# Kernel optimization log

Measured on AMD Instinct MI355X. Metric: run time of the kernel, lower is better.

## Reference

```python
import jax, jax.numpy as jnp
import numpy as np

B, H, SQ, SKV, D, TOPK = 1, 16, 1024, 4096, 128, 64


def setup_inputs() -> dict:
    key = jax.random.key(0)
    kq, kk, kv, ki, ks = jax.random.split(key, 5)
    q = jax.random.normal(kq, (B, H, SQ, D), dtype=jnp.float32)
    k = jax.random.normal(kk, (B, H, SKV, D), dtype=jnp.float32)
    v = jax.random.normal(kv, (B, H, SKV, D), dtype=jnp.float32)
    topk_indices = jax.random.randint(ki, (B, SQ, TOPK), 0, SKV, dtype=jnp.int32)
    topk_scores = jax.random.uniform(ks, (B, SQ, TOPK), dtype=jnp.float32)
    return {"q": q, "k": k, "v": v, "topk_indices": topk_indices,
            "topk_scores": topk_scores}


def reference(q, k, v, topk_indices, topk_scores):
    # q: (b,h,s,d); k,v: (b,h,S,d) global (cp_world_size=1 all-gather is identity)
    head_dim = q.shape[-1]
    scale = head_dim ** -0.5
    # Gather selected K/V per query without dense (b,h,s,S,d) expansion.
    # idx: (b,1,s,topk,1) broadcast against (b,h,1,S,d) along axis=3.
    idx = topk_indices[:, None, :, :, None]
    k_g = jnp.take_along_axis(k[:, :, None, :, :], idx, axis=3)  # (b,h,s,t,d)
    v_g = jnp.take_along_axis(v[:, :, None, :, :], idx, axis=3)  # (b,h,s,t,d)
    scores = jnp.einsum("bhsd,bhstd->bhst", q, k_g) * scale
    w = jax.nn.softmax(scores, axis=-1)
    # rescale by indexer scores and renormalize
    w = w * topk_scores[:, None, :, :]
    w = w / (jnp.sum(w, axis=-1, keepdims=True) + 1e-12)
    out = jnp.einsum("bhst,bhstd->bhsd", w, v_g)
    return out
```

## Files before the change

kernel.cpp:

```cpp
#include <hip/hip_runtime.h>
#include <hip/hip_fp16.h>

#define NH  16
#define SQL 1024
#define SKV 4096
#define HD  128
#define TK  64

typedef _Float16 h2_t  __attribute__((ext_vector_type(2)));
typedef float    f32x4 __attribute__((ext_vector_type(4)));

__device__ __forceinline__ unsigned pkh(float x, float y) {
    return (unsigned)__half_as_ushort(__float2half(x)) |
           ((unsigned)__half_as_ushort(__float2half(y)) << 16);
}

__global__ __launch_bounds__(256) void cvt_f16_xcd(
    const float* __restrict__ k, const float* __restrict__ v,
    unsigned short* __restrict__ kh, unsigned short* __restrict__ vh)
{
    const int b   = blockIdx.x;
    const int xcd = b & 7;
    const int j   = b >> 3;
    const int isK = j >> 8;
    const int hsel= (j >> 7) & 1;
    const int chk = j & 127;
    const int h   = xcd | (hsel << 3);

    const float*    src = isK ? k  : v;
    unsigned short* dst = isK ? kh : vh;
    const size_t base = (size_t)h * SKV * HD + (size_t)chk * 4096
                      + (size_t)threadIdx.x * 16;
    const float4* s4 = (const float4*)(src + base);
    uint4*        d4 = (uint4*)(dst + base);
#pragma unroll
    for (int u = 0; u < 2; ++u) {
        float4 a = s4[2 * u], c = s4[2 * u + 1];
        uint4 o;
        o.x = pkh(a.x, a.y);
        o.y = pkh(a.z, a.w);
        o.z = pkh(c.x, c.y);
        o.w = pkh(c.z, c.w);
        d4[u] = o;
    }
}

__global__ __launch_bounds__(256) void dsa_f16p(
    const float* __restrict__ q, const unsigned short* __restrict__ kh,
    const unsigned short* __restrict__ vh, const int* __restrict__ tidx,
    const float* __restrict__ tsc, float* __restrict__ out)
{
    __shared__ float scr[4][TK][17];

    const int tid  = threadIdx.x;
    const int wv   = tid >> 6;
    const int lane = tid & 63;
    const int quad = lane >> 4;
    const int l16  = lane & 15;
    const int bi   = blockIdx.x;
    const int xcd  = bi & 7;
    const int s0   = (bi >> 3) * 4 + wv;

    const int   tIdx = tidx[s0 * TK + lane];
    const float tSc  = tsc[s0 * TK + lane];

    for (int rnd = 0; rnd < 2; ++rnd) {
        const int h = xcd | (rnd << 3);
        const unsigned short* kb = kh + (size_t)h * SKV * HD;
        const unsigned short* vb = vh + (size_t)h * SKV * HD;

        const float* qp = q + (size_t)(h * SQL + s0) * HD + 8 * l16;
        const f32x4 qa = __builtin_nontemporal_load((const f32x4*)qp);
        const f32x4 qb = __builtin_nontemporal_load((const f32x4*)qp + 1);
        h2_t q0 = {(_Float16)qa.x, (_Float16)qa.y};
        h2_t q1 = {(_Float16)qa.z, (_Float16)qa.w};
        h2_t q2 = {(_Float16)qb.x, (_Float16)qb.y};
        h2_t q3 = {(_Float16)qb.z, (_Float16)qb.w};

        float part[16];
#pragma unroll
        for (int i = 0; i < 16; ++i) {
            const size_t row = (size_t)__shfl(tIdx, 4 * i + quad);
            uint4 kw = *(const uint4*)(kb + row * HD + 8 * l16);
            float d = 0.f;
#if __has_builtin(__builtin_amdgcn_fdot2)
            d = __builtin_amdgcn_fdot2(q0, __builtin_bit_cast(h2_t, kw.x), d, false);
            d = __builtin_amdgcn_fdot2(q1, __builtin_bit_cast(h2_t, kw.y), d, false);
            d = __builtin_amdgcn_fdot2(q2, __builtin_bit_cast(h2_t, kw.z), d, false);
            d = __builtin_amdgcn_fdot2(q3, __builtin_bit_cast(h2_t, kw.w), d, false);
#else
            {
                float2 k0 = __half22float2(__builtin_bit_cast(__half2, kw.x));
                float2 k1 = __half22float2(__builtin_bit_cast(__half2, kw.y));
                float2 k2 = __half22float2(__builtin_bit_cast(__half2, kw.z));
                float2 k3 = __half22float2(__builtin_bit_cast(__half2, kw.w));
                d  = qa.x * k0.x + qa.y * k0.y + qa.z * k1.x + qa.w * k1.y;
                d += qb.x * k2.x + qb.y * k2.y + qb.z * k3.x + qb.w * k3.y;
            }
#endif
            part[i] = d;
        }

#pragma unroll
        for (int i = 0; i < 16; ++i) scr[wv][4 * i + quad][l16] = part[i];
        float acc = 0.f;
#pragma unroll
        for (int m = 0; m < 16; ++m) acc += scr[wv][lane][m];
        acc *= 0.08838834764831845f;

        float mx = acc;
#pragma unroll
        for (int off = 32; off; off >>= 1) mx = fmaxf(mx, __shfl_xor(mx, off));
        const float e   = __expf(acc - mx);
        const float ets = e * tSc;
        float se = e, sets = ets;
#pragma unroll
        for (int off = 32; off; off >>= 1) {
            se   += __shfl_xor(se, off);
            sets += __shfl_xor(sets, off);
        }
        const float w = ets / (sets + 1e-12f * se);
        const unsigned wpk = __builtin_bit_cast(unsigned, __float2half2_rn(w));

        __syncthreads();

        __half2 o0 = __float2half2_rn(0.f);
        __half2 o1 = o0, o2 = o0, o3 = o0;
#pragma unroll
        for (int i = 0; i < 16; ++i) {
            const size_t row = (size_t)__shfl(tIdx, 4 * i + quad);
            uint4 vw = *(const uint4*)(vb + row * HD + 8 * l16);
            const __half2 w2 = __builtin_bit_cast(__half2, __shfl(wpk, 4 * i + quad));
            o0 = __hfma2(w2, __builtin_bit_cast(__half2, vw.x), o0);
            o1 = __hfma2(w2, __builtin_bit_cast(__half2, vw.y), o1);
            o2 = __hfma2(w2, __builtin_bit_cast(__half2, vw.z), o2);
            o3 = __hfma2(w2, __builtin_bit_cast(__half2, vw.w), o3);
        }

        __half2 oo[4] = {o0, o1, o2, o3};
#pragma unroll
        for (int j = 0; j < 4; ++j) {
            unsigned u = __builtin_bit_cast(unsigned, oo[j]);
            oo[j] = __hadd2(oo[j], __builtin_bit_cast(__half2, __shfl_xor(u, 16)));
            u = __builtin_bit_cast(unsigned, oo[j]);
            oo[j] = __hadd2(oo[j], __builtin_bit_cast(__half2, __shfl_xor(u, 32)));
        }

        if (quad == 0) {
            float2 f0 = __half22float2(oo[0]);
            float2 f1 = __half22float2(oo[1]);
            float2 f2 = __half22float2(oo[2]);
            float2 f3 = __half22float2(oo[3]);
            float* op = out + (size_t)(h * SQL + s0) * HD + 8 * l16;
            f32x4 w0 = {f0.x, f0.y, f1.x, f1.y};
            f32x4 w1 = {f2.x, f2.y, f3.x, f3.y};
            __builtin_nontemporal_store(w0, (f32x4*)op);
            __builtin_nontemporal_store(w1, (f32x4*)op + 1);
        }

        if (rnd == 0) __syncthreads();
    }
}

__global__ __launch_bounds__(256) void dsa_fp32(
    const float* __restrict__ q, const float* __restrict__ k,
    const float* __restrict__ v, const int* __restrict__ tidx,
    const float* __restrict__ tsc, float* __restrict__ out)
{
    __shared__ int   idxs[4][TK];
    __shared__ float wsc[4][TK];
    const int tid = threadIdx.x, wv = tid >> 6, lane = tid & 63;
    const int half = lane >> 5, l32 = lane & 31, bi = blockIdx.x;
    const int h = ((bi & 7) << 1) | ((bi >> 3) & 1);
    const int s = ((bi >> 4) << 2) + wv;
    const float* qp = q + (size_t)(h * SQL + s) * HD;
    const float4 qf = *(const float4*)(qp + 4 * l32);
    const float t_sc = tsc[s * TK + lane];
    idxs[wv][lane] = tidx[s * TK + lane];
    const float* kb = k + (size_t)h * SKV * HD;
#pragma unroll 4
    for (int i = 0; i < TK / 2; ++i) {
        const int t = 2 * i + half, row = idxs[wv][t];
        float4 k4 = *(const float4*)(kb + (size_t)row * HD + 4 * l32);
        float d = k4.x * qf.x + k4.y * qf.y + k4.z * qf.z + k4.w * qf.w;
        d += __shfl_xor(d, 16); d += __shfl_xor(d, 8); d += __shfl_xor(d, 4);
        d += __shfl_xor(d, 2);  d += __shfl_xor(d, 1);
        if (l32 == 0) wsc[wv][t] = d;
    }
    float acc = wsc[wv][lane] * 0.08838834764831845f;
    float m = acc;
#pragma unroll
    for (int off = 32; off; off >>= 1) m = fmaxf(m, __shfl_xor(m, off));
    const float e = __expf(acc - m), ets = e * t_sc;
    float se = e, sets = ets;
#pragma unroll
    for (int off = 32; off; off >>= 1) { se += __shfl_xor(se, off); sets += __shfl_xor(sets, off); }
    wsc[wv][lane] = ets / (sets + 1e-12f * se);
    const float* vbp = v + (size_t)h * SKV * HD;
    float4 o = make_float4(0.f, 0.f, 0.f, 0.f);
#pragma unroll 4
    for (int i = 0; i < TK / 2; ++i) {
        const int t = 2 * i + half, row = idxs[wv][t];
        const float wt = wsc[wv][t];
        float4 v4 = *(const float4*)(vbp + (size_t)row * HD + 4 * l32);
        o.x += wt * v4.x; o.y += wt * v4.y; o.z += wt * v4.z; o.w += wt * v4.w;
    }
    o.x += __shfl_xor(o.x, 32); o.y += __shfl_xor(o.y, 32);
    o.z += __shfl_xor(o.z, 32); o.w += __shfl_xor(o.w, 32);
    if (half == 0) *(float4*)(out + (size_t)(h * SQL + s) * HD + 4 * l32) = o;
}

extern "C" void kernel_launch(void* const* d_in, const int* in_sizes, int n_in,
                              void* d_out, int out_size, void* d_ws, size_t ws_size,
                              hipStream_t stream) {
    const float* q  = (const float*)d_in[0];
    const float* k  = (const float*)d_in[1];
    const float* v  = (const float*)d_in[2];
    const int*   ti = (const int*)d_in[3];
    const float* ts = (const float*)d_in[4];
    float* out = (float*)d_out;

    const size_t nkv  = (size_t)NH * SKV * HD;
    const size_t need = 2 * nkv * sizeof(unsigned short);
    if (ws_size >= need) {
        unsigned short* kh = (unsigned short*)d_ws;
        unsigned short* vh = kh + nkv;
        cvt_f16_xcd<<<dim3(4096), dim3(256), 0, stream>>>(k, v, kh, vh);
        dsa_f16p<<<dim3(2048), dim3(256), 0, stream>>>(q, kh, vh, ti, ts, out);
    } else {
        dsa_fp32<<<dim3(4096), dim3(256), 0, stream>>>(q, k, v, ti, ts, out);
    }
}
```

Before: 137.2 us.

## Overlap fp16 conversion of upper heads with attention via grid-wide barrier

The first kernel now converts K/V to fp16 only for heads 0-7. The attention kernel processes two queries per wave on those heads while converting the K/V slice for heads 8-15 in the same blocks, then waits on a global atomic counter barrier before attending over heads 8-15. This hides most of the conversion cost behind attention work and halves the standalone conversion launch. It also prefetches all V rows into registers before the softmax. The spin barrier depends on all 1024 blocks being co-resident, which launch_bounds(256,4) is meant to ensure; the barrier has a spin-count timeout, so results could be wrong if residency fails.

```diff
diff --git a/kernel.cpp b/kernel.cpp
--- a/kernel.cpp
+++ b/kernel.cpp
@@ -1,11 +1,12 @@
 #include <hip/hip_runtime.h>
 #include <hip/hip_fp16.h>
 
-#define NH  16
-#define SQL 1024
-#define SKV 4096
-#define HD  128
-#define TK  64
+#define NH   16
+#define SQL  1024
+#define SKV  4096
+#define HD   128
+#define TK   64
+#define NBLK 1024
 
 typedef _Float16 h2_t  __attribute__((ext_vector_type(2)));
 typedef float    f32x4 __attribute__((ext_vector_type(4)));
@@ -15,27 +16,27 @@
            ((unsigned)__half_as_ushort(__float2half(y)) << 16);
 }
 
-__global__ __launch_bounds__(256) void cvt_f16_xcd(
+__global__ __launch_bounds__(256) void cvt_r0(
     const float* __restrict__ k, const float* __restrict__ v,
-    unsigned short* __restrict__ kh, unsigned short* __restrict__ vh)
+    unsigned short* __restrict__ kh, unsigned short* __restrict__ vh,
+    unsigned* ctr)
 {
+    if (blockIdx.x == 0 && threadIdx.x == 0) *ctr = 0u;
     const int b   = blockIdx.x;
-    const int xcd = b & 7;
+    const int x   = b & 7;
     const int j   = b >> 3;
-    const int isK = j >> 8;
-    const int hsel= (j >> 7) & 1;
-    const int chk = j & 127;
-    const int h   = xcd | (hsel << 3);
-
+    const int isK = j >> 7;
+    const int sl  = j & 127;
     const float*    src = isK ? k  : v;
     unsigned short* dst = isK ? kh : vh;
-    const size_t base = (size_t)h * SKV * HD + (size_t)chk * 4096
+    const size_t base = (size_t)x * SKV * HD + (size_t)sl * 4096
                       + (size_t)threadIdx.x * 16;
-    const float4* s4 = (const float4*)(src + base);
-    uint4*        d4 = (uint4*)(dst + base);
+    const f32x4* s4 = (const f32x4*)(src + base);
+    uint4*       d4 = (uint4*)(dst + base);
 #pragma unroll
     for (int u = 0; u < 2; ++u) {
-        float4 a = s4[2 * u], c = s4[2 * u + 1];
+        f32x4 a = __builtin_nontemporal_load(s4 + 2 * u);
+        f32x4 c = __builtin_nontemporal_load(s4 + 2 * u + 1);
         uint4 o;
         o.x = pkh(a.x, a.y);
         o.y = pkh(a.z, a.w);
@@ -45,10 +46,111 @@
     }
 }
 
-__global__ __launch_bounds__(256) void dsa_f16p(
-    const float* __restrict__ q, const unsigned short* __restrict__ kh,
-    const unsigned short* __restrict__ vh, const int* __restrict__ tidx,
-    const float* __restrict__ tsc, float* __restrict__ out)
+__device__ __forceinline__ void attn_one(
+    const float* __restrict__ q, const unsigned short* __restrict__ kb,
+    const unsigned short* __restrict__ vb, float* __restrict__ out,
+    int h, int s, int tIdx, float tSc,
+    float (*scrw)[17], int lane, int quad, int l16)
+{
+    const float* qp = q + (size_t)(h * SQL + s) * HD + 8 * l16;
+    const f32x4 qa = __builtin_nontemporal_load((const f32x4*)qp);
+    const f32x4 qb = __builtin_nontemporal_load((const f32x4*)qp + 1);
+    h2_t q0 = {(_Float16)qa.x, (_Float16)qa.y};
+    h2_t q1 = {(_Float16)qa.z, (_Float16)qa.w};
+    h2_t q2 = {(_Float16)qb.x, (_Float16)qb.y};
+    h2_t q3 = {(_Float16)qb.z, (_Float16)qb.w};
+
+    float part[16];
+#pragma unroll
+    for (int i = 0; i < 16; ++i) {
+        const size_t row = (size_t)__shfl(tIdx, 4 * i + quad);
+        uint4 kw = *(const uint4*)(kb + row * HD + 8 * l16);
+        float d = 0.f;
+#if __has_builtin(__builtin_amdgcn_fdot2)
+        d = __builtin_amdgcn_fdot2(q0, __builtin_bit_cast(h2_t, kw.x), d, false);
+        d = __builtin_amdgcn_fdot2(q1, __builtin_bit_cast(h2_t, kw.y), d, false);
+        d = __builtin_amdgcn_fdot2(q2, __builtin_bit_cast(h2_t, kw.z), d, false);
+        d = __builtin_amdgcn_fdot2(q3, __builtin_bit_cast(h2_t, kw.w), d, false);
+#else
+        {
+            float2 k0 = __half22float2(__builtin_bit_cast(__half2, kw.x));
+            float2 k1 = __half22float2(__builtin_bit_cast(__half2, kw.y));
+            float2 k2 = __half22float2(__builtin_bit_cast(__half2, kw.z));
+            float2 k3 = __half22float2(__builtin_bit_cast(__half2, kw.w));
+            d  = qa.x * k0.x + qa.y * k0.y + qa.z * k1.x + qa.w * k1.y;
+            d += qb.x * k2.x + qb.y * k2.y + qb.z * k3.x + qb.w * k3.y;
+        }
+#endif
+        part[i] = d;
+    }
+
+    uint4 vw[16];
+#pragma unroll
+    for (int i = 0; i < 16; ++i) {
+        const size_t row = (size_t)__shfl(tIdx, 4 * i + quad);
+        vw[i] = *(const uint4*)(vb + row * HD + 8 * l16);
+    }
+
+#pragma unroll
+    for (int i = 0; i < 16; ++i) scrw[4 * i + quad][l16] = part[i];
+    float acc = 0.f;
+#pragma unroll
+    for (int m = 0; m < 16; ++m) acc += scrw[lane][m];
+    acc *= 0.08838834764831845f;
+
+    float mx = acc;
+#pragma unroll
+    for (int off = 32; off; off >>= 1) mx = fmaxf(mx, __shfl_xor(mx, off));
+    const float e   = __expf(acc - mx);
+    const float ets = e * tSc;
+    float se = e, sets = ets;
+#pragma unroll
+    for (int off = 32; off; off >>= 1) {
+        se   += __shfl_xor(se, off);
+        sets += __shfl_xor(sets, off);
+    }
+    const float w = ets / (sets + 1e-12f * se);
+    const unsigned wpk = __builtin_bit_cast(unsigned, __float2half2_rn(w));
+
+    __half2 o0 = __float2half2_rn(0.f);
+    __half2 o1 = o0, o2 = o0, o3 = o0;
+#pragma unroll
+    for (int i = 0; i < 16; ++i) {
+        const __half2 w2 = __builtin_bit_cast(__half2, __shfl(wpk, 4 * i + quad));
+        o0 = __hfma2(w2, __builtin_bit_cast(__half2, vw[i].x), o0);
+        o1 = __hfma2(w2, __builtin_bit_cast(__half2, vw[i].y), o1);
+        o2 = __hfma2(w2, __builtin_bit_cast(__half2, vw[i].z), o2);
+        o3 = __hfma2(w2, __builtin_bit_cast(__half2, vw[i].w), o3);
+    }
+
+    __half2 oo[4] = {o0, o1, o2, o3};
+#pragma unroll
+    for (int j = 0; j < 4; ++j) {
+        unsigned u = __builtin_bit_cast(unsigned, oo[j]);
+        oo[j] = __hadd2(oo[j], __builtin_bit_cast(__half2, __shfl_xor(u, 16)));
+        u = __builtin_bit_cast(unsigned, oo[j]);
+        oo[j] = __hadd2(oo[j], __builtin_bit_cast(__half2, __shfl_xor(u, 32)));
+    }
+
+    if (quad == 0) {
+        float2 f0 = __half22float2(oo[0]);
+        float2 f1 = __half22float2(oo[1]);
+        float2 f2 = __half22float2(oo[2]);
+        float2 f3 = __half22float2(oo[3]);
+        float* op = out + (size_t)(h * SQL + s) * HD + 8 * l16;
+        f32x4 w0 = {f0.x, f0.y, f1.x, f1.y};
+        f32x4 w1 = {f2.x, f2.y, f3.x, f3.y};
+        __builtin_nontemporal_store(w0, (f32x4*)op);
+        __builtin_nontemporal_store(w1, (f32x4*)op + 1);
+    }
+}
+
+__global__ __launch_bounds__(256, 4) void dsa_ov(
+    const float* __restrict__ q, const float* __restrict__ k,
+    const float* __restrict__ v, const int* __restrict__ tidx,
+    const float* __restrict__ tsc, float* __restrict__ out,
+    unsigned short* __restrict__ kh, unsigned short* __restrict__ vh,
+    unsigned* ctr)
 {
     __shared__ float scr[4][TK][17];
 
@@ -58,108 +160,78 @@
     const int quad = lane >> 4;
     const int l16  = lane & 15;
     const int bi   = blockIdx.x;
-    const int xcd  = bi & 7;
-    const int s0   = (bi >> 3) * 4 + wv;
-
-    const int   tIdx = tidx[s0 * TK + lane];
-    const float tSc  = tsc[s0 * TK + lane];
-
-    for (int rnd = 0; rnd < 2; ++rnd) {
-        const int h = xcd | (rnd << 3);
-        const unsigned short* kb = kh + (size_t)h * SKV * HD;
-        const unsigned short* vb = vh + (size_t)h * SKV * HD;
-
-        const float* qp = q + (size_t)(h * SQL + s0) * HD + 8 * l16;
-        const f32x4 qa = __builtin_nontemporal_load((const f32x4*)qp);
-        const f32x4 qb = __builtin_nontemporal_load((const f32x4*)qp + 1);
-        h2_t q0 = {(_Float16)qa.x, (_Float16)qa.y};
-        h2_t q1 = {(_Float16)qa.z, (_Float16)qa.w};
-        h2_t q2 = {(_Float16)qb.x, (_Float16)qb.y};
-        h2_t q3 = {(_Float16)qb.z, (_Float16)qb.w};
-
-        float part[16];
-#pragma unroll
-        for (int i = 0; i < 16; ++i) {
-            const size_t row = (size_t)__shfl(tIdx, 4 * i + quad);
-            uint4 kw = *(const uint4*)(kb + row * HD + 8 * l16);
-            float d = 0.f;
-#if __has_builtin(__builtin_amdgcn_fdot2)
-            d = __builtin_amdgcn_fdot2(q0, __builtin_bit_cast(h2_t, kw.x), d, false);
-            d = __builtin_amdgcn_fdot2(q1, __builtin_bit_cast(h2_t, kw.y), d, false);
-            d = __builtin_amdgcn_fdot2(q2, __builtin_bit_cast(h2_t, kw.z), d, false);
-            d = __builtin_amdgcn_fdot2(q3, __builtin_bit_cast(h2_t, kw.w), d, false);
-#else
-            {
-                float2 k0 = __half22float2(__builtin_bit_cast(__half2, kw.x));
-                float2 k1 = __half22float2(__builtin_bit_cast(__half2, kw.y));
-                float2 k2 = __half22float2(__builtin_bit_cast(__half2, kw.z));
-                float2 k3 = __half22float2(__builtin_bit_cast(__half2, kw.w));
-                d  = qa.x * k0.x + qa.y * k0.y + qa.z * k1.x + qa.w * k1.y;
-                d += qb.x * k2.x + qb.y * k2.y + qb.z * k3.x + qb.w * k3.y;
-            }
-#endif
-            part[i] = d;
+    const int x    = bi & 7;
+    const int blkx = bi >> 3;
+    const int s0   = blkx * 8 + wv * 2;
+
+    int   tIdx[2];
+    float tSc[2];
+#pragma unroll
+    for (int qi = 0; qi < 2; ++qi) {
+        tIdx[qi] = tidx[(s0 + qi) * TK + lane];
+        tSc[qi]  = tsc[(s0 + qi) * TK + lane];
+    }
+
+    const int h8 = x | 8;
+    const size_t cbase = (size_t)h8 * SKV * HD + (size_t)blkx * 4096
+                       + (size_t)tid * 16;
+
+    const unsigned short* kb0 = kh + (size_t)x * SKV * HD;
+    const unsigned short* vb0 = vh + (size_t)x * SKV * HD;
+
+    attn_one(q, kb0, vb0, out, x, s0, tIdx[0], tSc[0], scr[wv], lane, quad, l16);
+
+    const f32x4* ks4 = (const f32x4*)(k + cbase);
+    f32x4 ck0 = __builtin_nontemporal_load(ks4);
+    f32x4 ck1 = __builtin_nontemporal_load(ks4 + 1);
+    f32x4 ck2 = __builtin_nontemporal_load(ks4 + 2);
+    f32x4 ck3 = __builtin_nontemporal_load(ks4 + 3);
+
+    attn_one(q, kb0, vb0, out, x, s0 + 1, tIdx[1], tSc[1], scr[wv], lane, quad, l16);
+
+    {
+        uint4* d4 = (uint4*)(kh + cbase);
+        uint4 o0, o1;
+        o0.x = pkh(ck0.x, ck0.y); o0.y = pkh(ck0.z, ck0.w);
+        o0.z = pkh(ck1.x, ck1.y); o0.w = pkh(ck1.z, ck1.w);
+        o1.x = pkh(ck2.x, ck2.y); o1.y = pkh(ck2.z, ck2.w);
+        o1.z = pkh(ck3.x, ck3.y); o1.w = pkh(ck3.z, ck3.w);
+        d4[0] = o0; d4[1] = o1;
+    }
+    {
+        const f32x4* vs4 = (const f32x4*)(v + cbase);
+        f32x4 a0 = __builtin_nontemporal_load(vs4);
+        f32x4 a1 = __builtin_nontemporal_load(vs4 + 1);
+        f32x4 a2 = __builtin_nontemporal_load(vs4 + 2);
+        f32x4 a3 = __builtin_nontemporal_load(vs4 + 3);
+        uint4* d4 = (uint4*)(vh + cbase);
+        uint4 o0, o1;
+        o0.x = pkh(a0.x, a0.y); o0.y = pkh(a0.z, a0.w);
+        o0.z = pkh(a1.x, a1.y); o0.w = pkh(a1.z, a1.w);
+        o1.x = pkh(a2.x, a2.y); o1.y = pkh(a2.z, a2.w);
+        o1.z = pkh(a3.x, a3.y); o1.w = pkh(a3.z, a3.w);
+        d4[0] = o0; d4[1] = o1;
+    }
+
+    __syncthreads();
+    if (tid == 0) {
+        __threadfence();
+        __hip_atomic_fetch_add(ctr, 1u, __ATOMIC_ACQ_REL,
+                               __HIP_MEMORY_SCOPE_AGENT);
+        int spins = 0;
+        while (__hip_atomic_load(ctr, __ATOMIC_ACQUIRE,
+                                 __HIP_MEMORY_SCOPE_AGENT) < (unsigned)NBLK) {
+            __builtin_amdgcn_s_sleep(8);
+            if (++spins > 100000) break;
         }
-
-#pragma unroll
-        for (int i = 0; i < 16; ++i) scr[wv][4 * i + quad][l16] = part[i];
-        float acc = 0.f;
-#pragma unroll
-        for (int m = 0; m < 16; ++m) acc += scr[wv][lane][m];
-        acc *= 0.08838834764831845f;
-
-        float mx = acc;
-#pragma unroll
-        for (int off = 32; off; off >>= 1) mx = fmaxf(mx, __shfl_xor(mx, off));
-        const float e   = __expf(acc - mx);
-        const float ets = e * tSc;
-        float se = e, sets = ets;
-#pragma unroll
-        for (int off = 32; off; off >>= 1) {
-            se   += __shfl_xor(se, off);
-            sets += __shfl_xor(sets, off);
-        }
-        const float w = ets / (sets + 1e-12f * se);
-        const unsigned wpk = __builtin_bit_cast(unsigned, __float2half2_rn(w));
-
-        __syncthreads();
-
-        __half2 o0 = __float2half2_rn(0.f);
-        __half2 o1 = o0, o2 = o0, o3 = o0;
-#pragma unroll
-        for (int i = 0; i < 16; ++i) {
-            const size_t row = (size_t)__shfl(tIdx, 4 * i + quad);
-            uint4 vw = *(const uint4*)(vb + row * HD + 8 * l16);
-            const __half2 w2 = __builtin_bit_cast(__half2, __shfl(wpk, 4 * i + quad));
-            o0 = __hfma2(w2, __builtin_bit_cast(__half2, vw.x), o0);
-            o1 = __hfma2(w2, __builtin_bit_cast(__half2, vw.y), o1);
-            o2 = __hfma2(w2, __builtin_bit_cast(__half2, vw.z), o2);
-            o3 = __hfma2(w2, __builtin_bit_cast(__half2, vw.w), o3);
-        }
-
-        __half2 oo[4] = {o0, o1, o2, o3};
-#pragma unroll
-        for (int j = 0; j < 4; ++j) {
-            unsigned u = __builtin_bit_cast(unsigned, oo[j]);
-            oo[j] = __hadd2(oo[j], __builtin_bit_cast(__half2, __shfl_xor(u, 16)));
-            u = __builtin_bit_cast(unsigned, oo[j]);
-            oo[j] = __hadd2(oo[j], __builtin_bit_cast(__half2, __shfl_xor(u, 32)));
-        }
-
-        if (quad == 0) {
-            float2 f0 = __half22float2(oo[0]);
-            float2 f1 = __half22float2(oo[1]);
-            float2 f2 = __half22float2(oo[2]);
-            float2 f3 = __half22float2(oo[3]);
-            float* op = out + (size_t)(h * SQL + s0) * HD + 8 * l16;
-            f32x4 w0 = {f0.x, f0.y, f1.x, f1.y};
-            f32x4 w1 = {f2.x, f2.y, f3.x, f3.y};
-            __builtin_nontemporal_store(w0, (f32x4*)op);
-            __builtin_nontemporal_store(w1, (f32x4*)op + 1);
-        }
-
-        if (rnd == 0) __syncthreads();
-    }
+        __threadfence();
+    }
+    __syncthreads();
+
+    const unsigned short* kb1 = kh + (size_t)h8 * SKV * HD;
+    const unsigned short* vb1 = vh + (size_t)h8 * SKV * HD;
+    attn_one(q, kb1, vb1, out, h8, s0,     tIdx[0], tSc[0], scr[wv], lane, quad, l16);
+    attn_one(q, kb1, vb1, out, h8, s0 + 1, tIdx[1], tSc[1], scr[wv], lane, quad, l16);
 }
 
 __global__ __launch_bounds__(256) void dsa_fp32(
@@ -220,13 +292,17 @@
     const float* ts = (const float*)d_in[4];
     float* out = (float*)d_out;
 
-    const size_t nkv  = (size_t)NH * SKV * HD;
-    const size_t need = 2 * nkv * sizeof(unsigned short);
+    const size_t nkv   = (size_t)NH * SKV * HD;
+    const size_t fp16b = 2 * nkv * sizeof(unsigned short);
+    const size_t need  = fp16b + 256;
     if (ws_size >= need) {
         unsigned short* kh = (unsigned short*)d_ws;
         unsigned short* vh = kh + nkv;
-        cvt_f16_xcd<<<dim3(4096), dim3(256), 0, stream>>>(k, v, kh, vh);
-        dsa_f16p<<<dim3(2048), dim3(256), 0, stream>>>(q, kh, vh, ti, ts, out);
+        unsigned* ctr = (unsigned*)((char*)d_ws + fp16b);
+
+        cvt_r0<<<dim3(2048), dim3(256), 0, stream>>>(k, v, kh, vh, ctr);
+        dsa_ov<<<dim3(NBLK), dim3(256), 0, stream>>>(q, k, v, ti, ts, out,
+                                                     kh, vh, ctr);
     } else {
         dsa_fp32<<<dim3(4096), dim3(256), 0, stream>>>(q, k, v, ti, ts, out);
     }
```

After: 382.3 us. +178.6%, slower.
